# Performance work log

Measured on AMD Instinct MI355X. Metric: run time of the kernel, lower is better.

Reference implementation:

```python
import jax, jax.numpy as jnp
import numpy as np

B, H, LQ, LK, D, HID = 2, 1, 512, 512, 64, 128


def setup_inputs() -> dict:
    key = jax.random.key(0)
    ks = jax.random.split(key, 8)
    f = lambda k, shape, s=1.0: jax.random.normal(k, shape, dtype=jnp.float32) * s
    return {
        "q": f(ks[0], (B, H, LQ, D)),
        "k": f(ks[1], (B, H, LK, D)),
        "v": f(ks[2], (B, H, LK, D)),
        "mask": jnp.zeros((B, H, LQ, LK), jnp.float32),
        # shared q/k/v projection (self.w) and output projection (self.dense)
        "Ww": f(ks[3], (D, D), 0.1), "wb": jnp.zeros((D,), jnp.float32),
        "Wd": f(ks[4], (D, D), 0.1), "db": jnp.zeros((D,), jnp.float32),
        # two-layer MLP NN: 2*D -> HID -> 1
        "W1": f(ks[5], (2 * D, HID), 0.1), "b1": jnp.zeros((HID,), jnp.float32),
        "W2": f(ks[6], (HID, 1), 0.1), "b2": jnp.zeros((1,), jnp.float32),
    }


def _sim_scores(q, k, W1, b1, W2, b2, make_sym):
    # Equivalent to tile+concat+MLP, but splits W1 so the 2*D concat tensor
    # is never materialized; only the [B,H,Lq,Lk,HID] hidden is.
    W1q, W1k = W1[:D], W1[D:]
    qa = q @ W1q  # [B,H,Lq,HID]
    kb = k @ W1k  # [B,H,Lk,HID]
    h = jax.nn.relu(qa[:, :, :, None, :] + kb[:, :, None, :, :] + b1)
    s = (h @ W2)[..., 0] + b2[0]  # [B,H,Lq,Lk]
    if make_sym:
        # concat([k, q]) order: hidden2 = relu(k_j @ W1q + q_i @ W1k + b1)
        qb = q @ W1k
        ka = k @ W1q
        h2 = jax.nn.relu(qb[:, :, :, None, :] + ka[:, :, None, :, :] + b1)
        s = s + (h2 @ W2)[..., 0] + b2[0]
    return s


def reference(q, k, v, mask, Ww, wb, Wd, db, W1, b1, W2, b2):
    make_sym = True
    qp = q @ Ww + wb
    kp = k @ Ww + wb
    vp = v @ Ww + wb
    logits = _sim_scores(qp, kp, W1, b1, W2, b2, make_sym)
    logits = logits + mask * (-1e9)
    attn = jax.nn.softmax(logits, axis=-1)  # [B,H,Lq,Lk]
    out = attn @ vp                          # [B,H,Lq,D]
    out = out @ Wd + db
    return (out, attn)
```

## Files before the change

kernel.cpp:

```cpp
#include <hip/hip_runtime.h>
#include <hip/hip_bf16.h>


#define NROWS 1024
#define DD    64
#define HH    128
#define LK_   512
#define QR    4

__global__ __launch_bounds__(128)
void proj_kernel(const float* __restrict__ q, const float* __restrict__ k,
                 const float* __restrict__ v,
                 const float* __restrict__ Ww, const float* __restrict__ wb,
                 const float* __restrict__ W1, const float* __restrict__ b1,
                 const float* __restrict__ Wd,
                 float* __restrict__ vpd,
                 float* __restrict__ qa, float* __restrict__ qb,
                 float* __restrict__ kaTf, float* __restrict__ kbTf)
{
    const int r    = blockIdx.x;
    const int type = r >> 10;
    const int idx  = r & 1023;
    const int t    = threadIdx.x;

    const float* src = (type == 0) ? q : (type == 1) ? k : v;

    __shared__ float x[DD];
    __shared__ float xp[DD];

    if (t < DD) x[t] = src[idx * DD + t];
    __syncthreads();

    if (t < DD) {
        float acc = wb[t];
        #pragma unroll
        for (int c = 0; c < DD; ++c) acc = fmaf(x[c], Ww[c * DD + t], acc);
        xp[t] = acc;
    }
    __syncthreads();

    if (type == 2) {
        if (t < DD) {
            float acc = 0.f;
            #pragma unroll
            for (int c = 0; c < DD; ++c) acc = fmaf(xp[c], Wd[c * DD + t], acc);
            vpd[idx * DD + t] = acc;
        }
        return;
    }

    float accA = 0.f;
    float accB = 0.f;
    #pragma unroll
    for (int d = 0; d < DD; ++d) {
        const float xv = xp[d];
        accA = fmaf(xv, W1[d * HH + t],        accA);
        accB = fmaf(xv, W1[(DD + d) * HH + t], accB);
    }
    if (type == 0) {
        qa[idx * HH + t] = accA + b1[t];
        qb[idx * HH + t] = accB + b1[t];
    } else {
        const int b  = idx >> 9;
        const int j  = idx & (LK_ - 1);
        const int o  = ((b * (HH / 4) + (t >> 2)) * LK_ + j) * 4 + (t & 3);
        kaTf[o] = accA;
        kbTf[o] = accB;
    }
}

__global__ __launch_bounds__(512)
void attn_kernel(const float* __restrict__ mask,
                 const float* __restrict__ vpd,
                 const float* __restrict__ qa, const float* __restrict__ qb,
                 const float4* __restrict__ kaT, const float4* __restrict__ kbT,
                 const float* __restrict__ W2, const float* __restrict__ b2,
                 const float* __restrict__ db,
                 float* __restrict__ out, float* __restrict__ attn)
{
    const int row0 = blockIdx.x * QR;
    const int b    = row0 >> 9;
    const int t    = threadIdx.x;
    const int wid  = t >> 6;
    const int lane = t & 63;
    const int j    = t;

    __shared__ float redm[8][QR];
    __shared__ float reds[8][QR];
    __shared__ float opart[8][QR][DD];

    const float4* kaTb = kaT + b * (HH / 4) * LK_;
    const float4* kbTb = kbT + b * (HH / 4) * LK_;
    const float*  qaR  = qa + row0 * HH;
    const float*  qbR  = qb + row0 * HH;
    const float4* w24  = reinterpret_cast<const float4*>(W2);

    float mk[QR];
    #pragma unroll
    for (int r = 0; r < QR; ++r) mk[r] = mask[(row0 + r) * LK_ + j];

    float s1[QR] = {0.f, 0.f, 0.f, 0.f};
    float s2[QR] = {0.f, 0.f, 0.f, 0.f};
    #pragma unroll 2
    for (int h4 = 0; h4 < HH / 4; ++h4) {
        const float4 w   = w24[h4];
        const float4 kb4 = kbTb[h4 * LK_ + j];
        const float4 ka4 = kaTb[h4 * LK_ + j];
        const int h = h4 * 4;
        #pragma unroll
        for (int r = 0; r < QR; ++r) {
            s1[r] = fmaf(fmaxf(qaR[r * HH + h + 0] + kb4.x, 0.f), w.x, s1[r]);
            s1[r] = fmaf(fmaxf(qaR[r * HH + h + 1] + kb4.y, 0.f), w.y, s1[r]);
            s1[r] = fmaf(fmaxf(qaR[r * HH + h + 2] + kb4.z, 0.f), w.z, s1[r]);
            s1[r] = fmaf(fmaxf(qaR[r * HH + h + 3] + kb4.w, 0.f), w.w, s1[r]);
            s2[r] = fmaf(fmaxf(qbR[r * HH + h + 0] + ka4.x, 0.f), w.x, s2[r]);
            s2[r] = fmaf(fmaxf(qbR[r * HH + h + 1] + ka4.y, 0.f), w.y, s2[r]);
            s2[r] = fmaf(fmaxf(qbR[r * HH + h + 2] + ka4.z, 0.f), w.z, s2[r]);
            s2[r] = fmaf(fmaxf(qbR[r * HH + h + 3] + ka4.w, 0.f), w.w, s2[r]);
        }
    }

    const float b2v = b2[0];
    float sv[QR];
    #pragma unroll
    for (int r = 0; r < QR; ++r)
        sv[r] = s1[r] + s2[r] + 2.f * b2v + mk[r] * (-1e9f);

    float m[QR];
    #pragma unroll
    for (int r = 0; r < QR; ++r) {
        float mv = sv[r];
        #pragma unroll
        for (int off = 32; off > 0; off >>= 1) mv = fmaxf(mv, __shfl_xor(mv, off));
        if (lane == 0) redm[wid][r] = mv;
    }
    __syncthreads();
    #pragma unroll
    for (int r = 0; r < QR; ++r) {
        float mv = redm[0][r];
        #pragma unroll
        for (int w = 1; w < 8; ++w) mv = fmaxf(mv, redm[w][r]);
        m[r] = mv;
    }

    float e[QR];
    #pragma unroll
    for (int r = 0; r < QR; ++r) {
        e[r] = expf(sv[r] - m[r]);
        float s = e[r];
        #pragma unroll
        for (int off = 32; off > 0; off >>= 1) s += __shfl_xor(s, off);
        if (lane == 0) reds[wid][r] = s;
    }
    __syncthreads();

    float pv[QR];
    #pragma unroll
    for (int r = 0; r < QR; ++r) {
        float s = reds[0][r];
        #pragma unroll
        for (int w = 1; w < 8; ++w) s += reds[w][r];
        pv[r] = e[r] / s;
        attn[(row0 + r) * LK_ + j] = pv[r];
    }

    float acc[QR] = {0.f, 0.f, 0.f, 0.f};
    {
        const int jb = wid * 64;
        const float* vb = vpd + (b * LK_ + jb) * DD;
        #pragma unroll
        for (int jj = 0; jj < 64; ++jj) {
            const float vv = vb[jj * DD + lane];
            #pragma unroll
            for (int r = 0; r < QR; ++r) {
                const float pj = __int_as_float(
                    __builtin_amdgcn_readlane(__float_as_int(pv[r]), jj));
                acc[r] = fmaf(pj, vv, acc[r]);
            }
        }
    }
    #pragma unroll
    for (int r = 0; r < QR; ++r) opart[wid][r][lane] = acc[r];
    __syncthreads();

    if (t < QR * DD) {
        const int r = t >> 6, d = t & 63;
        float o = opart[0][r][d];
        #pragma unroll
        for (int w = 1; w < 8; ++w) o += opart[w][r][d];
        out[(row0 + r) * DD + d] = o + db[d];
    }
}

extern "C" void kernel_launch(void* const* d_in, const int* in_sizes, int n_in,
                              void* d_out, int out_size, void* d_ws, size_t ws_size,
                              hipStream_t stream)
{
    const float* q    = (const float*)d_in[0];
    const float* k    = (const float*)d_in[1];
    const float* v    = (const float*)d_in[2];
    const float* mask = (const float*)d_in[3];
    const float* Ww   = (const float*)d_in[4];
    const float* wb   = (const float*)d_in[5];
    const float* Wd   = (const float*)d_in[6];
    const float* db   = (const float*)d_in[7];
    const float* W1   = (const float*)d_in[8];
    const float* b1   = (const float*)d_in[9];
    const float* W2   = (const float*)d_in[10];
    const float* b2   = (const float*)d_in[11];

    float* ws = (float*)d_ws;
    float* vpd = ws;
    float* qa  = vpd + NROWS * DD;
    float* qb  = qa + NROWS * HH;
    float* kaTf = qb + NROWS * HH;
    float* kbTf = kaTf + NROWS * HH;

    float* out  = (float*)d_out;
    float* attn = out + NROWS * DD;

    proj_kernel<<<dim3(3072), dim3(128), 0, stream>>>(
        q, k, v, Ww, wb, W1, b1, Wd, vpd, qa, qb, kaTf, kbTf);

    attn_kernel<<<dim3(NROWS / QR), dim3(512), 0, stream>>>(
        mask, vpd, qa, qb, (const float4*)kaTf, (const float4*)kbTf,
        W2, b2, db, out, attn);
}
```

Baseline: 103.1 us.

## Remap attn threads to 2 rows x 2 keys to reuse q loads, stage probs in LDS

Each thread now computes two query rows for two key columns, not four rows for one key, so every q value it loads is reused across two keys. Softmax reductions are split per half-block and use a reciprocal multiply instead of a divide. Probabilities are written to shared memory in a row-interleaved layout and read back as float4 for the PV product, replacing per-element readlane broadcasts. The cost is an extra barrier, more shared memory and twice the k loads per thread.

```diff
diff --git a/kernel.cpp b/kernel.cpp
--- a/kernel.cpp
+++ b/kernel.cpp
@@ -83,100 +83,128 @@
     const int t    = threadIdx.x;
     const int wid  = t >> 6;
     const int lane = t & 63;
-    const int j    = t;
-
-    __shared__ float redm[8][QR];
-    __shared__ float reds[8][QR];
+    const int rp   = t >> 8;
+    const int j1   = t & 255;
+    const int j2   = j1 + 256;
+
+    __shared__ float p_int[LK_ * QR];
+    __shared__ float redm[8][2];
+    __shared__ float reds[8][2];
     __shared__ float opart[8][QR][DD];
 
     const float4* kaTb = kaT + b * (HH / 4) * LK_;
     const float4* kbTb = kbT + b * (HH / 4) * LK_;
-    const float*  qaR  = qa + row0 * HH;
-    const float*  qbR  = qb + row0 * HH;
+    const float*  qaR  = qa + (row0 + 2 * rp) * HH;
+    const float*  qbR  = qb + (row0 + 2 * rp) * HH;
     const float4* w24  = reinterpret_cast<const float4*>(W2);
 
-    float mk[QR];
-    #pragma unroll
-    for (int r = 0; r < QR; ++r) mk[r] = mask[(row0 + r) * LK_ + j];
-
-    float s1[QR] = {0.f, 0.f, 0.f, 0.f};
-    float s2[QR] = {0.f, 0.f, 0.f, 0.f};
+    float mk[2][2];
+    #pragma unroll
+    for (int r = 0; r < 2; ++r) {
+        mk[r][0] = mask[(row0 + 2 * rp + r) * LK_ + j1];
+        mk[r][1] = mask[(row0 + 2 * rp + r) * LK_ + j2];
+    }
+
+    float s1[2][2] = {{0.f, 0.f}, {0.f, 0.f}};
+    float s2[2][2] = {{0.f, 0.f}, {0.f, 0.f}};
     #pragma unroll 2
     for (int h4 = 0; h4 < HH / 4; ++h4) {
-        const float4 w   = w24[h4];
-        const float4 kb4 = kbTb[h4 * LK_ + j];
-        const float4 ka4 = kaTb[h4 * LK_ + j];
+        const float4 w    = w24[h4];
+        const float4 kb4a = kbTb[h4 * LK_ + j1];
+        const float4 ka4a = kaTb[h4 * LK_ + j1];
+        const float4 kb4b = kbTb[h4 * LK_ + j2];
+        const float4 ka4b = kaTb[h4 * LK_ + j2];
         const int h = h4 * 4;
         #pragma unroll
-        for (int r = 0; r < QR; ++r) {
-            s1[r] = fmaf(fmaxf(qaR[r * HH + h + 0] + kb4.x, 0.f), w.x, s1[r]);
-            s1[r] = fmaf(fmaxf(qaR[r * HH + h + 1] + kb4.y, 0.f), w.y, s1[r]);
-            s1[r] = fmaf(fmaxf(qaR[r * HH + h + 2] + kb4.z, 0.f), w.z, s1[r]);
-            s1[r] = fmaf(fmaxf(qaR[r * HH + h + 3] + kb4.w, 0.f), w.w, s1[r]);
-            s2[r] = fmaf(fmaxf(qbR[r * HH + h + 0] + ka4.x, 0.f), w.x, s2[r]);
-            s2[r] = fmaf(fmaxf(qbR[r * HH + h + 1] + ka4.y, 0.f), w.y, s2[r]);
-            s2[r] = fmaf(fmaxf(qbR[r * HH + h + 2] + ka4.z, 0.f), w.z, s2[r]);
-            s2[r] = fmaf(fmaxf(qbR[r * HH + h + 3] + ka4.w, 0.f), w.w, s2[r]);
+        for (int r = 0; r < 2; ++r) {
+            const float qa0 = qaR[r * HH + h + 0], qa1 = qaR[r * HH + h + 1];
+            const float qa2 = qaR[r * HH + h + 2], qa3 = qaR[r * HH + h + 3];
+            const float qb0 = qbR[r * HH + h + 0], qb1 = qbR[r * HH + h + 1];
+            const float qb2 = qbR[r * HH + h + 2], qb3 = qbR[r * HH + h + 3];
+            s1[r][0] = fmaf(fmaxf(qa0 + kb4a.x, 0.f), w.x, s1[r][0]);
+            s1[r][0] = fmaf(fmaxf(qa1 + kb4a.y, 0.f), w.y, s1[r][0]);
+            s1[r][0] = fmaf(fmaxf(qa2 + kb4a.z, 0.f), w.z, s1[r][0]);
+            s1[r][0] = fmaf(fmaxf(qa3 + kb4a.w, 0.f), w.w, s1[r][0]);
+            s1[r][1] = fmaf(fmaxf(qa0 + kb4b.x, 0.f), w.x, s1[r][1]);
+            s1[r][1] = fmaf(fmaxf(qa1 + kb4b.y, 0.f), w.y, s1[r][1]);
+            s1[r][1] = fmaf(fmaxf(qa2 + kb4b.z, 0.f), w.z, s1[r][1]);
+            s1[r][1] = fmaf(fmaxf(qa3 + kb4b.w, 0.f), w.w, s1[r][1]);
+            s2[r][0] = fmaf(fmaxf(qb0 + ka4a.x, 0.f), w.x, s2[r][0]);
+            s2[r][0] = fmaf(fmaxf(qb1 + ka4a.y, 0.f), w.y, s2[r][0]);
+            s2[r][0] = fmaf(fmaxf(qb2 + ka4a.z, 0.f), w.z, s2[r][0]);
+            s2[r][0] = fmaf(fmaxf(qb3 + ka4a.w, 0.f), w.w, s2[r][0]);
+            s2[r][1] = fmaf(fmaxf(qb0 + ka4b.x, 0.f), w.x, s2[r][1]);
+            s2[r][1] = fmaf(fmaxf(qb1 + ka4b.y, 0.f), w.y, s2[r][1]);
+            s2[r][1] = fmaf(fmaxf(qb2 + ka4b.z, 0.f), w.z, s2[r][1]);
+            s2[r][1] = fmaf(fmaxf(qb3 + ka4b.w, 0.f), w.w, s2[r][1]);
         }
     }
 
     const float b2v = b2[0];
-    float sv[QR];
-    #pragma unroll
-    for (int r = 0; r < QR; ++r)
-        sv[r] = s1[r] + s2[r] + 2.f * b2v + mk[r] * (-1e9f);
-
-    float m[QR];
-    #pragma unroll
-    for (int r = 0; r < QR; ++r) {
-        float mv = sv[r];
+    float sv[2][2];
+    #pragma unroll
+    for (int r = 0; r < 2; ++r) {
+        sv[r][0] = s1[r][0] + s2[r][0] + 2.f * b2v + mk[r][0] * (-1e9f);
+        sv[r][1] = s1[r][1] + s2[r][1] + 2.f * b2v + mk[r][1] * (-1e9f);
+    }
+
+    float m[2];
+    #pragma unroll
+    for (int r = 0; r < 2; ++r) {
+        float mv = fmaxf(sv[r][0], sv[r][1]);
         #pragma unroll
         for (int off = 32; off > 0; off >>= 1) mv = fmaxf(mv, __shfl_xor(mv, off));
         if (lane == 0) redm[wid][r] = mv;
     }
     __syncthreads();
     #pragma unroll
-    for (int r = 0; r < QR; ++r) {
-        float mv = redm[0][r];
-        #pragma unroll
-        for (int w = 1; w < 8; ++w) mv = fmaxf(mv, redm[w][r]);
-        m[r] = mv;
-    }
-
-    float e[QR];
-    #pragma unroll
-    for (int r = 0; r < QR; ++r) {
-        e[r] = expf(sv[r] - m[r]);
-        float s = e[r];
+    for (int r = 0; r < 2; ++r) {
+        const int g = 4 * rp;
+        m[r] = fmaxf(fmaxf(redm[g][r], redm[g + 1][r]),
+                     fmaxf(redm[g + 2][r], redm[g + 3][r]));
+    }
+
+    float e[2][2];
+    #pragma unroll
+    for (int r = 0; r < 2; ++r) {
+        e[r][0] = expf(sv[r][0] - m[r]);
+        e[r][1] = expf(sv[r][1] - m[r]);
+        float s = e[r][0] + e[r][1];
         #pragma unroll
         for (int off = 32; off > 0; off >>= 1) s += __shfl_xor(s, off);
         if (lane == 0) reds[wid][r] = s;
     }
     __syncthreads();
 
-    float pv[QR];
-    #pragma unroll
-    for (int r = 0; r < QR; ++r) {
-        float s = reds[0][r];
-        #pragma unroll
-        for (int w = 1; w < 8; ++w) s += reds[w][r];
-        pv[r] = e[r] / s;
-        attn[(row0 + r) * LK_ + j] = pv[r];
-    }
+    float pv[2][2];
+    #pragma unroll
+    for (int r = 0; r < 2; ++r) {
+        const int g = 4 * rp;
+        const float s = reds[g][r] + reds[g + 1][r] + reds[g + 2][r] + reds[g + 3][r];
+        const float inv = 1.f / s;
+        pv[r][0] = e[r][0] * inv;
+        pv[r][1] = e[r][1] * inv;
+        attn[(row0 + 2 * rp + r) * LK_ + j1] = pv[r][0];
+        attn[(row0 + 2 * rp + r) * LK_ + j2] = pv[r][1];
+    }
+    *reinterpret_cast<float2*>(&p_int[j1 * QR + 2 * rp]) =
+        make_float2(pv[0][0], pv[1][0]);
+    *reinterpret_cast<float2*>(&p_int[j2 * QR + 2 * rp]) =
+        make_float2(pv[0][1], pv[1][1]);
+    __syncthreads();
 
     float acc[QR] = {0.f, 0.f, 0.f, 0.f};
     {
         const int jb = wid * 64;
         const float* vb = vpd + (b * LK_ + jb) * DD;
-        #pragma unroll
+        #pragma unroll 8
         for (int jj = 0; jj < 64; ++jj) {
+            const float4 pj = *reinterpret_cast<const float4*>(&p_int[(jb + jj) * QR]);
             const float vv = vb[jj * DD + lane];
-            #pragma unroll
-            for (int r = 0; r < QR; ++r) {
-                const float pj = __int_as_float(
-                    __builtin_amdgcn_readlane(__float_as_int(pv[r]), jj));
-                acc[r] = fmaf(pj, vv, acc[r]);
-            }
+            acc[0] = fmaf(pj.x, vv, acc[0]);
+            acc[1] = fmaf(pj.y, vv, acc[1]);
+            acc[2] = fmaf(pj.z, vv, acc[2]);
+            acc[3] = fmaf(pj.w, vv, acc[3]);
         }
     }
     #pragma unroll
```

Result: no change. 104.4 us (+1.3%).

## Split attention rows across 1024 threads and share probabilities via LDS

Applied to the files above, without the earlier changes.

Each attention block now runs 1024 threads, and each half of the block scores two of the four query rows instead of one thread scoring all four. That halves the per-thread MLP work and raises parallelism, since the grid is only 256 blocks. The probabilities are staged in shared memory so the P·V product can split keys across 16 waves, replacing the cross-lane readlane broadcast. The cost is an extra barrier, more LDS use and register pressure from the larger launch bound.

```diff
diff --git a/kernel.cpp b/kernel.cpp
--- a/kernel.cpp
+++ b/kernel.cpp
@@ -69,7 +69,7 @@
     }
 }
 
-__global__ __launch_bounds__(512)
+__global__ __launch_bounds__(1024)
 void attn_kernel(const float* __restrict__ mask,
                  const float* __restrict__ vpd,
                  const float* __restrict__ qa, const float* __restrict__ qb,
@@ -83,24 +83,26 @@
     const int t    = threadIdx.x;
     const int wid  = t >> 6;
     const int lane = t & 63;
-    const int j    = t;
-
-    __shared__ float redm[8][QR];
-    __shared__ float reds[8][QR];
-    __shared__ float opart[8][QR][DD];
+    const int rp   = t >> 9;
+    const int j    = t & (LK_ - 1);
+
+    __shared__ float p_int[LK_ * QR];
+    __shared__ float redm[16][2];
+    __shared__ float reds[16][2];
+    __shared__ float opart[16][QR][DD];
 
     const float4* kaTb = kaT + b * (HH / 4) * LK_;
     const float4* kbTb = kbT + b * (HH / 4) * LK_;
-    const float*  qaR  = qa + row0 * HH;
-    const float*  qbR  = qb + row0 * HH;
+    const float*  qaR  = qa + (row0 + 2 * rp) * HH;
+    const float*  qbR  = qb + (row0 + 2 * rp) * HH;
     const float4* w24  = reinterpret_cast<const float4*>(W2);
 
-    float mk[QR];
-    #pragma unroll
-    for (int r = 0; r < QR; ++r) mk[r] = mask[(row0 + r) * LK_ + j];
-
-    float s1[QR] = {0.f, 0.f, 0.f, 0.f};
-    float s2[QR] = {0.f, 0.f, 0.f, 0.f};
+    float mk[2];
+    #pragma unroll
+    for (int r = 0; r < 2; ++r) mk[r] = mask[(row0 + 2 * rp + r) * LK_ + j];
+
+    float s1[2] = {0.f, 0.f};
+    float s2[2] = {0.f, 0.f};
     #pragma unroll 2
     for (int h4 = 0; h4 < HH / 4; ++h4) {
         const float4 w   = w24[h4];
@@ -108,7 +110,7 @@
         const float4 ka4 = kaTb[h4 * LK_ + j];
         const int h = h4 * 4;
         #pragma unroll
-        for (int r = 0; r < QR; ++r) {
+        for (int r = 0; r < 2; ++r) {
             s1[r] = fmaf(fmaxf(qaR[r * HH + h + 0] + kb4.x, 0.f), w.x, s1[r]);
             s1[r] = fmaf(fmaxf(qaR[r * HH + h + 1] + kb4.y, 0.f), w.y, s1[r]);
             s1[r] = fmaf(fmaxf(qaR[r * HH + h + 2] + kb4.z, 0.f), w.z, s1[r]);
@@ -121,31 +123,32 @@
     }
 
     const float b2v = b2[0];
-    float sv[QR];
-    #pragma unroll
-    for (int r = 0; r < QR; ++r)
+    float sv[2];
+    #pragma unroll
+    for (int r = 0; r < 2; ++r)
         sv[r] = s1[r] + s2[r] + 2.f * b2v + mk[r] * (-1e9f);
 
-    float m[QR];
-    #pragma unroll
-    for (int r = 0; r < QR; ++r) {
+    #pragma unroll
+    for (int r = 0; r < 2; ++r) {
         float mv = sv[r];
         #pragma unroll
         for (int off = 32; off > 0; off >>= 1) mv = fmaxf(mv, __shfl_xor(mv, off));
         if (lane == 0) redm[wid][r] = mv;
     }
     __syncthreads();
-    #pragma unroll
-    for (int r = 0; r < QR; ++r) {
-        float mv = redm[0][r];
-        #pragma unroll
-        for (int w = 1; w < 8; ++w) mv = fmaxf(mv, redm[w][r]);
+    float m[2];
+    #pragma unroll
+    for (int r = 0; r < 2; ++r) {
+        const int g = 8 * rp;
+        float mv = redm[g][r];
+        #pragma unroll
+        for (int w = 1; w < 8; ++w) mv = fmaxf(mv, redm[g + w][r]);
         m[r] = mv;
     }
 
-    float e[QR];
-    #pragma unroll
-    for (int r = 0; r < QR; ++r) {
+    float e[2];
+    #pragma unroll
+    for (int r = 0; r < 2; ++r) {
         e[r] = expf(sv[r] - m[r]);
         float s = e[r];
         #pragma unroll
@@ -154,29 +157,32 @@
     }
     __syncthreads();
 
-    float pv[QR];
-    #pragma unroll
-    for (int r = 0; r < QR; ++r) {
-        float s = reds[0][r];
-        #pragma unroll
-        for (int w = 1; w < 8; ++w) s += reds[w][r];
+    float pv[2];
+    #pragma unroll
+    for (int r = 0; r < 2; ++r) {
+        const int g = 8 * rp;
+        float s = reds[g][r];
+        #pragma unroll
+        for (int w = 1; w < 8; ++w) s += reds[g + w][r];
         pv[r] = e[r] / s;
-        attn[(row0 + r) * LK_ + j] = pv[r];
-    }
+        attn[(row0 + 2 * rp + r) * LK_ + j] = pv[r];
+    }
+    *reinterpret_cast<float2*>(&p_int[j * QR + 2 * rp]) =
+        make_float2(pv[0], pv[1]);
+    __syncthreads();
 
     float acc[QR] = {0.f, 0.f, 0.f, 0.f};
     {
-        const int jb = wid * 64;
+        const int jb = wid * 32;
         const float* vb = vpd + (b * LK_ + jb) * DD;
-        #pragma unroll
-        for (int jj = 0; jj < 64; ++jj) {
+        #pragma unroll 8
+        for (int jj = 0; jj < 32; ++jj) {
+            const float4 pj = *reinterpret_cast<const float4*>(&p_int[(jb + jj) * QR]);
             const float vv = vb[jj * DD + lane];
-            #pragma unroll
-            for (int r = 0; r < QR; ++r) {
-                const float pj = __int_as_float(
-                    __builtin_amdgcn_readlane(__float_as_int(pv[r]), jj));
-                acc[r] = fmaf(pj, vv, acc[r]);
-            }
+            acc[0] = fmaf(pj.x, vv, acc[0]);
+            acc[1] = fmaf(pj.y, vv, acc[1]);
+            acc[2] = fmaf(pj.z, vv, acc[2]);
+            acc[3] = fmaf(pj.w, vv, acc[3]);
         }
     }
     #pragma unroll
@@ -187,7 +193,7 @@
         const int r = t >> 6, d = t & 63;
         float o = opart[0][r][d];
         #pragma unroll
-        for (int w = 1; w < 8; ++w) o += opart[w][r][d];
+        for (int w = 1; w < 16; ++w) o += opart[w][r][d];
         out[(row0 + r) * DD + d] = o + db[d];
     }
 }
@@ -222,7 +228,7 @@
     proj_kernel<<<dim3(3072), dim3(128), 0, stream>>>(
         q, k, v, Ww, wb, W1, b1, Wd, vpd, qa, qb, kaTf, kbTf);
 
-    attn_kernel<<<dim3(NROWS / QR), dim3(512), 0, stream>>>(
+    attn_kernel<<<dim3(NROWS / QR), dim3(1024), 0, stream>>>(
         mask, vpd, qa, qb, (const float4*)kaTf, (const float4*)kbTf,
         W2, b2, db, out, attn);
 }
```

Result: slower. 111.6 us (+8.2%).
